# Optimization experiments

Hardware: AMD Instinct MI355X
Metric: run time of the kernel (lower is better)

Reference implementation:

```python
import jax, jax.numpy as jnp
import numpy as np
import math

B, L, D, H = 2, 2048, 1024, 16
DK = D // H


def setup_inputs() -> dict:
    key = jax.random.key(0)
    ks = jax.random.split(key, 11)
    s = 1.0 / math.sqrt(D)
    inp = {
        "query": jax.random.normal(ks[0], (B, L, D), jnp.float32),
        "key": jax.random.normal(ks[1], (B, L, D), jnp.float32),
        "value": jax.random.normal(ks[2], (B, L, D), jnp.float32),
        # mask == True (==1) means masked-out; causal mask over future positions
        "mask": jnp.triu(jnp.ones((L, L), dtype=bool), k=1),
        "Wq": jax.random.normal(ks[3], (D, D), jnp.float32) * s,
        "bq": jnp.zeros((D,), jnp.float32),
        "Wk": jax.random.normal(ks[4], (D, D), jnp.float32) * s,
        "bk": jnp.zeros((D,), jnp.float32),
        "Wv": jax.random.normal(ks[5], (D, D), jnp.float32) * s,
        "bv": jnp.zeros((D,), jnp.float32),
        "Wo": jax.random.normal(ks[6], (D, D), jnp.float32) * s,
        "bo": jnp.zeros((D,), jnp.float32),
    }
    return inp


def reference(query, key, value, mask, Wq, bq, Wk, bk, Wv, bv, Wo, bo):
    # Linear projections, then split heads: [B, L, D] -> [B, H, L, DK]
    def proj(x, W, b):
        return (x @ W.T + b).reshape(B, -1, H, DK).transpose(0, 2, 1, 3)

    Q = proj(query, Wq, bq)
    K = proj(key, Wk, bk)
    V = proj(value, Wv, bv)

    scale = 1.0 / math.sqrt(DK)
    scores = jnp.einsum("bhqd,bhkd->bhqk", Q, K) * scale  # [B,H,Lq,Lk]
    scores = jnp.where(mask, -jnp.inf, scores)
    attn = jax.nn.softmax(scores, axis=-1)  # dropout p=0 (eval mode)
    out = jnp.einsum("bhqk,bhkd->bhqd", attn, V)
    out = out.transpose(0, 2, 1, 3).reshape(B, -1, D)  # merge heads
    return out @ Wo.T + bo
```

## Files before the change

kernel.cpp:

```cpp
#include <hip/hip_runtime.h>
#include <hip/hip_bf16.h>
#include <math.h>

#define NL 2048
#define ND 1024

typedef __attribute__((ext_vector_type(8))) __bf16 bf16x8;
typedef __attribute__((ext_vector_type(4))) float f32x4;
typedef __attribute__((ext_vector_type(16))) float f32x16;
typedef __attribute__((ext_vector_type(4))) short short4v;
typedef __attribute__((ext_vector_type(2))) unsigned uint2v;
typedef __attribute__((ext_vector_type(4))) unsigned uint4v;

__device__ __forceinline__ short f2bf(float f) {
    union { float f; unsigned u; } v; v.f = f;
    unsigned u = v.u;
    u += 0x7FFF + ((u >> 16) & 1);
    return (short)(u >> 16);
}

__device__ __forceinline__ unsigned cvtpk2(float lo, float hi) {
    unsigned r;
    asm("v_cvt_pk_bf16_f32 %0, %1, %2" : "=v"(r) : "v"(lo), "v"(hi));
    return r;
}

__device__ __forceinline__ void gload16(const short* g, short* l) {
    __builtin_amdgcn_global_load_lds(
        (const __attribute__((address_space(1))) void*)g,
        (__attribute__((address_space(3))) void*)l, 16, 0, 0);
}

__global__ __launch_bounds__(256) void cvt_all(
    const float* __restrict__ q, const float* __restrict__ k, const float* __restrict__ v,
    const float* __restrict__ wq, const float* __restrict__ wk, const float* __restrict__ wv,
    short* __restrict__ xq, short* __restrict__ xk, short* __restrict__ xv,
    short* __restrict__ wbf) {
    const int bid = blockIdx.x;
    const float* src;
    short* dst;
    int blk;
    if (bid < 6144) {
        const int t = bid >> 11;
        src = t == 0 ? q : t == 1 ? k : v;
        dst = t == 0 ? xq : t == 1 ? xk : xv;
        blk = bid & 2047;
    } else {
        const int b2 = bid - 6144;
        const int t = b2 >> 9;
        src = t == 0 ? wq : t == 1 ? wk : wv;
        dst = wbf + (size_t)t * (1 << 20);
        blk = b2 & 511;
    }
    const int i = blk * 2048 + threadIdx.x * 8;
    f32x4 v0 = *(const f32x4*)&src[i];
    f32x4 v1 = *(const f32x4*)&src[i + 4];
    uint4v u = { cvtpk2(v0[0], v0[1]), cvtpk2(v0[2], v0[3]),
                 cvtpk2(v1[0], v1[1]), cvtpk2(v1[2], v1[3]) };
    *(uint4v*)&dst[i] = u;
}

__global__ __launch_bounds__(256) void cvt1(const float* __restrict__ src,
                                            short* __restrict__ dst) {
    const int i = blockIdx.x * 2048 + threadIdx.x * 8;
    f32x4 v0 = *(const f32x4*)&src[i];
    f32x4 v1 = *(const f32x4*)&src[i + 4];
    uint4v u = { cvtpk2(v0[0], v0[1]), cvtpk2(v0[2], v0[3]),
                 cvtpk2(v1[0], v1[1]), cvtpk2(v1[2], v1[3]) };
    *(uint4v*)&dst[i] = u;
}

__device__ __forceinline__ void gemm_core(const short* gA, const short* gB,
                                          short (*As)[4096], short (*Bs)[4096],
                                          int w, int wr, int wc, int lr, int lc,
                                          f32x4 acc[4][4]) {
    gload16(gA,         &As[0][w * 512]);
    gload16(gA + 65536, &As[0][w * 512 + 2048]);
    gload16(gB,         &Bs[0][w * 512]);
    gload16(gB + 65536, &Bs[0][w * 512 + 2048]);
    gload16(gA + 32,         &As[1][w * 512]);
    gload16(gA + 65536 + 32, &As[1][w * 512 + 2048]);
    gload16(gB + 32,         &Bs[1][w * 512]);
    gload16(gB + 65536 + 32, &Bs[1][w * 512 + 2048]);

    for (int t = 0; t < 30; ++t) {
        const int ws_ = (t + 2) & 3, rd = t & 3;
        const int k2 = (t + 2) * 32;
        gload16(gA + k2,         &As[ws_][w * 512]);
        gload16(gA + 65536 + k2, &As[ws_][w * 512 + 2048]);
        gload16(gB + k2,         &Bs[ws_][w * 512]);
        gload16(gB + 65536 + k2, &Bs[ws_][w * 512 + 2048]);
        asm volatile("s_waitcnt vmcnt(8)" ::: "memory");
        __builtin_amdgcn_s_barrier();
        asm volatile("" ::: "memory");

        bf16x8 a[4], b[4];
        #pragma unroll
        for (int mt = 0; mt < 4; ++mt)
            a[mt] = *(const bf16x8*)&As[rd][(wr * 64 + mt * 16 + lc) * 32 + lr * 8];
        #pragma unroll
        for (int nt = 0; nt < 4; ++nt)
            b[nt] = *(const bf16x8*)&Bs[rd][(wc * 64 + nt * 16 + lc) * 32 + lr * 8];
        __builtin_amdgcn_s_setprio(1);
        #pragma unroll
        for (int mt = 0; mt < 4; ++mt)
            #pragma unroll
            for (int nt = 0; nt < 4; ++nt)
                acc[mt][nt] = __builtin_amdgcn_mfma_f32_16x16x32_bf16(
                    a[mt], b[nt], acc[mt][nt], 0, 0, 0);
        __builtin_amdgcn_s_setprio(0);
    }
    #pragma unroll
    for (int pt = 0; pt < 2; ++pt) {
        if (pt == 0) asm volatile("s_waitcnt vmcnt(4)" ::: "memory");
        else         asm volatile("s_waitcnt vmcnt(0)" ::: "memory");
        __builtin_amdgcn_s_barrier();
        asm volatile("" ::: "memory");
        const int rd = 2 + pt;
        bf16x8 a[4], b[4];
        #pragma unroll
        for (int mt = 0; mt < 4; ++mt)
            a[mt] = *(const bf16x8*)&As[rd][(wr * 64 + mt * 16 + lc) * 32 + lr * 8];
        #pragma unroll
        for (int nt = 0; nt < 4; ++nt)
            b[nt] = *(const bf16x8*)&Bs[rd][(wc * 64 + nt * 16 + lc) * 32 + lr * 8];
        #pragma unroll
        for (int mt = 0; mt < 4; ++mt)
            #pragma unroll
            for (int nt = 0; nt < 4; ++nt)
                acc[mt][nt] = __builtin_amdgcn_mfma_f32_16x16x32_bf16(
                    a[mt], b[nt], acc[mt][nt], 0, 0, 0);
    }
}

__global__ __launch_bounds__(256) void gemm_qk(
    const short* __restrict__ Xqb, const short* __restrict__ Xkb,
    const short* __restrict__ Wqb, const short* __restrict__ Wkb,
    const float* __restrict__ bq, const float* __restrict__ bk,
    short* __restrict__ oq, short* __restrict__ ok) {
    __shared__ alignas(16) short As[4][4096];
    __shared__ alignas(16) short Bs[4][4096];

    const int bid  = blockIdx.x;
    const int xcd  = bid & 7, slot = bid >> 3;
    const int panel = xcd * 8 + (slot >> 3);
    const int zz   = panel >> 5;
    const int m0   = (panel & 31) * 128;
    const int n0   = (slot & 7) * 128;

    const short* Ab = zz ? Xkb : Xqb;
    const short* Wb = zz ? Wkb : Wqb;
    const float* bi = zz ? bk : bq;
    short* outp     = zz ? ok : oq;
    const float scl = zz ? 1.0f : 0.125f * 1.44269504088896f;

    const int tid = threadIdx.x, lane = tid & 63, w = tid >> 6;
    const int wr = w >> 1, wc = w & 1, lr = lane >> 4, lc = lane & 15;

    const short* gA = &Ab[(m0 + w * 16 + (lane >> 2)) * 1024 + (lane & 3) * 8];
    const short* gB = &Wb[(n0 + w * 16 + (lane >> 2)) * 1024 + (lane & 3) * 8];

    f32x4 acc[4][4] = {};
    gemm_core(gA, gB, As, Bs, w, wr, wc, lr, lc, acc);

    #pragma unroll
    for (int mt = 0; mt < 4; ++mt)
        #pragma unroll
        for (int nt = 0; nt < 4; ++nt)
            #pragma unroll
            for (int r = 0; r < 4; ++r) {
                int grow = m0 + wr * 64 + mt * 16 + lr * 4 + r;
                int gcol = n0 + wc * 64 + nt * 16 + lc;
                float val = (acc[mt][nt][r] + bi[gcol]) * scl;
                int bh = (grow >> 11) * 16 + (gcol >> 6);
                int q  = grow & 2047;
                int dk = gcol & 63;
                size_t addr = (size_t)bh * 131072 + (size_t)(q >> 5) * 2048 +
                              (dk >> 4) * 512 + ((dk >> 3) & 1) * 256 +
                              (q & 31) * 8 + (dk & 7);
                outp[addr] = f2bf(val);
            }
}

__global__ __launch_bounds__(256) void gemm_v(
    const short* __restrict__ Xvb, const short* __restrict__ Wvb,
    const float* __restrict__ bv, short* __restrict__ ov) {
    __shared__ alignas(16) short As[4][4096];
    __shared__ alignas(16) short Bs[4][4096];

    const int bid = blockIdx.x;
    const int xcd = bid & 7, slot = bid >> 3;
    const int m0  = (xcd * 4 + (slot >> 3)) * 128;
    const int n0  = (slot & 7) * 128;

    const int tid = threadIdx.x, lane = tid & 63, w = tid >> 6;
    const int wr = w >> 1, wc = w & 1, lr = lane >> 4, lc = lane & 15;

    const short* gA = &Xvb[(m0 + w * 16 + (lane >> 2)) * 1024 + (lane & 3) * 8];
    const short* gB = &Wvb[(n0 + w * 16 + (lane >> 2)) * 1024 + (lane & 3) * 8];

    f32x4 acc[4][4] = {};
    gemm_core(gA, gB, As, Bs, w, wr, wc, lr, lc, acc);

    #pragma unroll
    for (int mt = 0; mt < 4; ++mt)
        #pragma unroll
        for (int nt = 0; nt < 4; ++nt)
            #pragma unroll
            for (int r = 0; r < 4; ++r) {
                int grow = m0 + wr * 64 + mt * 16 + lr * 4 + r;
                int gcol = n0 + wc * 64 + nt * 16 + lc;
                float val = acc[mt][nt][r] + bv[gcol];
                int bh = (grow >> 11) * 16 + (gcol >> 6);
                int q  = grow & 2047;
                int dk = gcol & 63;
                size_t addr = (size_t)bh * 131072 + (size_t)(q >> 6) * 4096 +
                              ((q >> 4) & 3) * 1024 + (dk >> 5) * 512 +
                              ((q >> 3) & 1) * 256 + (dk & 31) * 8 + (q & 7);
                ov[addr] = f2bf(val);
            }
}

__global__ __launch_bounds__(256) void gemm_out(const short* __restrict__ Abf,
                                                const short* __restrict__ Wob,
                                                const float* __restrict__ bo,
                                                float* __restrict__ out) {
    __shared__ alignas(16) short As[4][4096];
    __shared__ alignas(16) short Bs[4][4096];

    const int bid = blockIdx.x;
    const int xcd = bid & 7, slot = bid >> 3;
    const int m0  = (xcd * 4 + (slot >> 3)) * 128;
    const int n0  = (slot & 7) * 128;

    const int tid = threadIdx.x, lane = tid & 63, w = tid >> 6;
    const int wr = w >> 1, wc = w & 1, lr = lane >> 4, lc = lane & 15;

    const short* gA = &Abf[(m0 + w * 16 + (lane >> 2)) * 1024 + (lane & 3) * 8];
    const short* gB = &Wob[(n0 + w * 16 + (lane >> 2)) * 1024 + (lane & 3) * 8];

    f32x4 acc[4][4] = {};
    gemm_core(gA, gB, As, Bs, w, wr, wc, lr, lc, acc);

    #pragma unroll
    for (int mt = 0; mt < 4; ++mt)
        #pragma unroll
        for (int nt = 0; nt < 4; ++nt)
            #pragma unroll
            for (int r = 0; r < 4; ++r) {
                int grow = m0 + wr * 64 + mt * 16 + lr * 4 + r;
                int gcol = n0 + wc * 64 + nt * 16 + lc;
                out[grow * 1024 + gcol] = acc[mt][nt][r] + bo[gcol];
            }
}

__global__ __launch_bounds__(256) void flash_attn(const short* __restrict__ Q,
                                                  const short* __restrict__ K,
                                                  const short* __restrict__ Vt,
                                                  short* __restrict__ AO) {
    __shared__ float mrg[2][64][49];

    const int tid  = threadIdx.x;
    const int lane = tid & 63;
    const int w    = tid >> 6;
    const int ql   = lane & 31;
    const int hi   = lane >> 5;

    const int bid  = blockIdx.x;
    const int xcd  = bid & 7;
    const int idx  = bid >> 3;
    const int bh   = xcd * 4 + (idx & 3);
    const int t    = 63 - (idx >> 2);
    const int q0   = t * 32;
    const int qa   = q0 + ql;
    const int nkb  = (t >> 1) + 1;
    const int kb_lo = (w * nkb) >> 2;
    const int kb_hi = ((w + 1) * nkb) >> 2;

    const short* Qp = Q  + (size_t)bh * 131072 + (size_t)t * 2048 + lane * 8;
    const short* Kp = K  + (size_t)bh * 131072 + lane * 8;
    const short* Vp = Vt + (size_t)bh * 131072 + lane * 8;

    bf16x8 qf[4];
    #pragma unroll
    for (int ks = 0; ks < 4; ++ks)
        qf[ks] = *(const bf16x8*)&Qp[ks * 512];

    f32x16 ot0 = {}, ot1 = {}, lacc = {};

    for (int kb = kb_lo; kb < kb_hi; ++kb) {
        bf16x8 kf[8];
        #pragma unroll
        for (int ks = 0; ks < 4; ++ks) {
            kf[2 * ks]     = *(const bf16x8*)&Kp[(size_t)(2 * kb) * 2048 + ks * 512];
            kf[2 * ks + 1] = *(const bf16x8*)&Kp[(size_t)(2 * kb + 1) * 2048 + ks * 512];
        }
        bf16x8 vf[8];
        #pragma unroll
        for (int ks = 0; ks < 4; ++ks) {
            vf[2 * ks]     = *(const bf16x8*)&Vp[(size_t)kb * 4096 + ks * 1024];
            vf[2 * ks + 1] = *(const bf16x8*)&Vp[(size_t)kb * 4096 + ks * 1024 + 512];
        }

        f32x16 st0 = {}, st1 = {};
        __builtin_amdgcn_s_setprio(1);
        #pragma unroll
        for (int ks = 0; ks < 4; ++ks) {
            st0 = __builtin_amdgcn_mfma_f32_32x32x16_bf16(kf[2 * ks],     qf[ks], st0, 0, 0, 0);
            st1 = __builtin_amdgcn_mfma_f32_32x32x16_bf16(kf[2 * ks + 1], qf[ks], st1, 0, 0, 0);
        }
        __builtin_amdgcn_s_setprio(0);

        if (kb == nkb - 1) {
            const int kv0 = kb * 64;
            #pragma unroll
            for (int r = 0; r < 16; ++r) {
                const int cr = (r & 3) + 8 * (r >> 2) + 4 * hi;
                if (kv0 + cr > qa)      st0[r] = -3.0e38f;
                if (kv0 + 32 + cr > qa) st1[r] = -3.0e38f;
            }
        }

        #pragma unroll
        for (int r = 0; r < 16; ++r) {
            st0[r] = exp2f(st0[r]);
            st1[r] = exp2f(st1[r]);
            lacc[r] += st0[r] + st1[r];
        }

        bf16x8 pf[4];
        #pragma unroll
        for (int blk = 0; blk < 2; ++blk) {
            const f32x16 s = blk ? st1 : st0;
            #pragma unroll
            for (int pks = 0; pks < 2; ++pks) {
                const int b = pks * 8;
                unsigned xa = cvtpk2(s[b + 0], s[b + 1]);
                unsigned xb = cvtpk2(s[b + 2], s[b + 3]);
                unsigned ya = cvtpk2(s[b + 4], s[b + 5]);
                unsigned yb = cvtpk2(s[b + 6], s[b + 7]);
                uint2v s0 = __builtin_amdgcn_permlane32_swap(xa, ya, false, false);
                uint2v s1 = __builtin_amdgcn_permlane32_swap(xb, yb, false, false);
                union { unsigned u[4]; bf16x8 v; } pu;
                pu.u[0] = s0[0]; pu.u[1] = s1[0]; pu.u[2] = s0[1]; pu.u[3] = s1[1];
                pf[blk * 2 + pks] = pu.v;
            }
        }

        __builtin_amdgcn_s_setprio(1);
        #pragma unroll
        for (int ks = 0; ks < 4; ++ks) {
            ot0 = __builtin_amdgcn_mfma_f32_32x32x16_bf16(vf[2 * ks],     pf[ks], ot0, 0, 0, 0);
            ot1 = __builtin_amdgcn_mfma_f32_32x32x16_bf16(vf[2 * ks + 1], pf[ks], ot1, 0, 0, 0);
        }
        __builtin_amdgcn_s_setprio(0);
    }

    if (w >= 2) {
        float* m = &mrg[w - 2][lane][0];
        #pragma unroll
        for (int r = 0; r < 16; ++r) {
            m[r] = ot0[r]; m[16 + r] = ot1[r]; m[32 + r] = lacc[r];
        }
    }
    __syncthreads();
    if (w < 2) {
        const float* m = &mrg[w][lane][0];
        #pragma unroll
        for (int r = 0; r < 16; ++r) {
            ot0[r] += m[r]; ot1[r] += m[16 + r]; lacc[r] += m[32 + r];
        }
    }
    if (w == 1) {
        float* m = &mrg[1][lane][0];
        #pragma unroll
        for (int r = 0; r < 16; ++r) {
            m[r] = ot0[r]; m[16 + r] = ot1[r]; m[32 + r] = lacc[r];
        }
    }
    __syncthreads();
    if (w == 0) {
        const float* m = &mrg[1][lane][0];
        #pragma unroll
        for (int r = 0; r < 16; ++r) {
            ot0[r] += m[r]; ot1[r] += m[16 + r]; lacc[r] += m[32 + r];
        }
        float sm[16];
        #pragma unroll
        for (int r = 0; r < 16; ++r) sm[r] = lacc[r];
        #pragma unroll
        for (int s = 8; s > 0; s >>= 1)
            #pragma unroll
            for (int i = 0; i < s; ++i) sm[i] += sm[i + s];
        const float l = sm[0] + __shfl_xor(sm[0], 32);
        const float inv = 1.f / l;

        const int b_ = bh >> 4, h_ = bh & 15;
        short* aoRow = AO + ((size_t)(b_ * NL + qa)) * ND + h_ * 64;
        #pragma unroll
        for (int db = 0; db < 2; ++db) {
            const f32x16 o = db ? ot1 : ot0;
            #pragma unroll
            for (int g = 0; g < 4; ++g) {
                short4v sv;
                #pragma unroll
                for (int i = 0; i < 4; ++i) sv[i] = f2bf(o[g * 4 + i] * inv);
                *(short4v*)&aoRow[db * 32 + g * 8 + 4 * hi] = sv;
            }
        }
    }
}

extern "C" void kernel_launch(void* const* d_in, const int* in_sizes, int n_in,
                              void* d_out, int out_size, void* d_ws, size_t ws_size,
                              hipStream_t stream) {
    const float* query = (const float*)d_in[0];
    const float* key   = (const float*)d_in[1];
    const float* value = (const float*)d_in[2];
    const float* Wq = (const float*)d_in[4];
    const float* bq = (const float*)d_in[5];
    const float* Wk = (const float*)d_in[6];
    const float* bk = (const float*)d_in[7];
    const float* Wv = (const float*)d_in[8];
    const float* bv = (const float*)d_in[9];
    const float* Wo = (const float*)d_in[10];
    const float* bo = (const float*)d_in[11];

    short* ws    = (short*)d_ws;
    short* dob   = (short*)d_out;
    short* q_ws  = ws;
    short* k_ws  = ws + (4 << 20);
    short* xq    = ws + (8 << 20);
    short* vt_ws = ws + (8 << 20);
    short* wbf   = ws + (12 << 20);
    short* ao_ws = ws + (12 << 20);
    short* wobf  = ws;
    short* xk    = dob;
    short* xv    = dob + (4 << 20);

    cvt_all<<<dim3(7680), 256, 0, stream>>>(query, key, value, Wq, Wk, Wv,
                                            xq, xk, xv, wbf);
    gemm_qk<<<dim3(512), 256, 0, stream>>>(xq, xk, wbf, wbf + (1 << 20),
                                           bq, bk, q_ws, k_ws);
    gemm_v<<<dim3(256), 256, 0, stream>>>(xv, wbf + (2 << 20), bv, vt_ws);
    flash_attn<<<dim3(2048), dim3(256), 0, stream>>>(q_ws, k_ws, vt_ws, ao_ws);
    cvt1<<<dim3(512), 256, 0, stream>>>(Wo, wobf);
    gemm_out<<<dim3(256), 256, 0, stream>>>(ao_ws, wobf, bo, (float*)d_out);
}
```

Baseline: 134.6 us.

## Split flash attention KV range over two waves with K double-buffering

```diff
diff --git a/kernel.cpp b/kernel.cpp
--- a/kernel.cpp
+++ b/kernel.cpp
@@ -254,11 +254,11 @@
             }
 }
 
-__global__ __launch_bounds__(256) void flash_attn(const short* __restrict__ Q,
-                                                  const short* __restrict__ K,
-                                                  const short* __restrict__ Vt,
-                                                  short* __restrict__ AO) {
-    __shared__ float mrg[2][64][49];
+__global__ __launch_bounds__(128, 3) void flash_attn(const short* __restrict__ Q,
+                                                     const short* __restrict__ K,
+                                                     const short* __restrict__ Vt,
+                                                     short* __restrict__ AO) {
+    __shared__ float mrg[64][49];
 
     const int tid  = threadIdx.x;
     const int lane = tid & 63;
@@ -274,8 +274,9 @@
     const int q0   = t * 32;
     const int qa   = q0 + ql;
     const int nkb  = (t >> 1) + 1;
-    const int kb_lo = (w * nkb) >> 2;
-    const int kb_hi = ((w + 1) * nkb) >> 2;
+    const int nkb2 = nkb >> 1;
+    const int kb_lo = w == 0 ? 0 : nkb2;
+    const int kb_hi = w == 0 ? nkb2 : nkb;
 
     const short* Qp = Q  + (size_t)bh * 131072 + (size_t)t * 2048 + lane * 8;
     const short* Kp = K  + (size_t)bh * 131072 + lane * 8;
@@ -288,102 +289,112 @@
 
     f32x16 ot0 = {}, ot1 = {}, lacc = {};
 
-    for (int kb = kb_lo; kb < kb_hi; ++kb) {
-        bf16x8 kf[8];
-        #pragma unroll
-        for (int ks = 0; ks < 4; ++ks) {
-            kf[2 * ks]     = *(const bf16x8*)&Kp[(size_t)(2 * kb) * 2048 + ks * 512];
-            kf[2 * ks + 1] = *(const bf16x8*)&Kp[(size_t)(2 * kb + 1) * 2048 + ks * 512];
-        }
-        bf16x8 vf[8];
-        #pragma unroll
-        for (int ks = 0; ks < 4; ++ks) {
-            vf[2 * ks]     = *(const bf16x8*)&Vp[(size_t)kb * 4096 + ks * 1024];
-            vf[2 * ks + 1] = *(const bf16x8*)&Vp[(size_t)kb * 4096 + ks * 1024 + 512];
-        }
-
-        f32x16 st0 = {}, st1 = {};
-        __builtin_amdgcn_s_setprio(1);
-        #pragma unroll
-        for (int ks = 0; ks < 4; ++ks) {
-            st0 = __builtin_amdgcn_mfma_f32_32x32x16_bf16(kf[2 * ks],     qf[ks], st0, 0, 0, 0);
-            st1 = __builtin_amdgcn_mfma_f32_32x32x16_bf16(kf[2 * ks + 1], qf[ks], st1, 0, 0, 0);
-        }
-        __builtin_amdgcn_s_setprio(0);
-
-        if (kb == nkb - 1) {
-            const int kv0 = kb * 64;
-            #pragma unroll
-            for (int r = 0; r < 16; ++r) {
-                const int cr = (r & 3) + 8 * (r >> 2) + 4 * hi;
-                if (kv0 + cr > qa)      st0[r] = -3.0e38f;
-                if (kv0 + 32 + cr > qa) st1[r] = -3.0e38f;
+#define LOADK(KF, KB)                                                          \
+    {                                                                          \
+        _Pragma("unroll")                                                      \
+        for (int ks = 0; ks < 4; ++ks) {                                       \
+            KF[2 * ks]     = *(const bf16x8*)&Kp[(size_t)(2 * (KB)) * 2048 + ks * 512];     \
+            KF[2 * ks + 1] = *(const bf16x8*)&Kp[(size_t)(2 * (KB) + 1) * 2048 + ks * 512]; \
+        }                                                                      \
+    }
+
+#define COMPUTE(KF, KB)                                                        \
+    {                                                                          \
+        f32x16 st0 = {}, st1 = {};                                             \
+        __builtin_amdgcn_s_setprio(1);                                         \
+        _Pragma("unroll")                                                      \
+        for (int ks = 0; ks < 4; ++ks) {                                       \
+            st0 = __builtin_amdgcn_mfma_f32_32x32x16_bf16(KF[2 * ks],     qf[ks], st0, 0, 0, 0); \
+            st1 = __builtin_amdgcn_mfma_f32_32x32x16_bf16(KF[2 * ks + 1], qf[ks], st1, 0, 0, 0); \
+        }                                                                      \
+        __builtin_amdgcn_s_setprio(0);                                         \
+        bf16x8 vf[8];                                                          \
+        _Pragma("unroll")                                                      \
+        for (int ks = 0; ks < 4; ++ks) {                                       \
+            vf[2 * ks]     = *(const bf16x8*)&Vp[(size_t)(KB) * 4096 + ks * 1024];       \
+            vf[2 * ks + 1] = *(const bf16x8*)&Vp[(size_t)(KB) * 4096 + ks * 1024 + 512]; \
+        }                                                                      \
+        if ((KB) == nkb - 1) {                                                 \
+            const int kv0 = (KB) * 64;                                         \
+            _Pragma("unroll")                                                  \
+            for (int r = 0; r < 16; ++r) {                                     \
+                const int cr = (r & 3) + 8 * (r >> 2) + 4 * hi;                \
+                if (kv0 + cr > qa)      st0[r] = -3.0e38f;                     \
+                if (kv0 + 32 + cr > qa) st1[r] = -3.0e38f;                     \
+            }                                                                  \
+        }                                                                      \
+        _Pragma("unroll")                                                      \
+        for (int r = 0; r < 16; ++r) {                                         \
+            st0[r] = exp2f(st0[r]);                                            \
+            st1[r] = exp2f(st1[r]);                                            \
+            lacc[r] += st0[r] + st1[r];                                        \
+        }                                                                      \
+        bf16x8 pf[4];                                                          \
+        _Pragma("unroll")                                                      \
+        for (int blk = 0; blk < 2; ++blk) {                                    \
+            const f32x16 s = blk ? st1 : st0;                                  \
+            _Pragma("unroll")                                                  \
+            for (int pks = 0; pks < 2; ++pks) {                                \
+                const int b = pks * 8;                                         \
+                unsigned xa = cvtpk2(s[b + 0], s[b + 1]);                      \
+                unsigned xb = cvtpk2(s[b + 2], s[b + 3]);                      \
+                unsigned ya = cvtpk2(s[b + 4], s[b + 5]);                      \
+                unsigned yb = cvtpk2(s[b + 6], s[b + 7]);                      \
+                uint2v s0 = __builtin_amdgcn_permlane32_swap(xa, ya, false, false); \
+                uint2v s1 = __builtin_amdgcn_permlane32_swap(xb, yb, false, false); \
+                union { unsigned u[4]; bf16x8 v; } pu;                         \
+                pu.u[0] = s0[0]; pu.u[1] = s1[0]; pu.u[2] = s0[1]; pu.u[3] = s1[1]; \
+                pf[blk * 2 + pks] = pu.v;                                      \
+            }                                                                  \
+        }                                                                      \
+        __builtin_amdgcn_s_setprio(1);                                         \
+        _Pragma("unroll")                                                      \
+        for (int ks = 0; ks < 4; ++ks) {                                       \
+            ot0 = __builtin_amdgcn_mfma_f32_32x32x16_bf16(vf[2 * ks],     pf[ks], ot0, 0, 0, 0); \
+            ot1 = __builtin_amdgcn_mfma_f32_32x32x16_bf16(vf[2 * ks + 1], pf[ks], ot1, 0, 0, 0); \
+        }                                                                      \
+        __builtin_amdgcn_s_setprio(0);                                         \
+    }
+
+    if (kb_lo < kb_hi) {
+        bf16x8 k0_[8], k1_[8];
+        int kb = kb_lo;
+        LOADK(k0_, kb);
+        while (kb + 1 < kb_hi) {
+            LOADK(k1_, kb + 1);
+            COMPUTE(k0_, kb);
+            ++kb;
+            if (kb + 1 < kb_hi) {
+                LOADK(k0_, kb + 1);
+                COMPUTE(k1_, kb);
+                ++kb;
+            } else {
+                COMPUTE(k1_, kb);
+                ++kb;
             }
         }
-
+        if (kb < kb_hi) {
+            COMPUTE(k0_, kb);
+        }
+    }
+#undef LOADK
+#undef COMPUTE
+
+    if (w == 0) {
         #pragma unroll
         for (int r = 0; r < 16; ++r) {
-            st0[r] = exp2f(st0[r]);
-            st1[r] = exp2f(st1[r]);
-            lacc[r] += st0[r] + st1[r];
+            mrg[lane][r]      = ot0[r];
+            mrg[lane][16 + r] = ot1[r];
+            mrg[lane][32 + r] = lacc[r];
         }
-
-        bf16x8 pf[4];
-        #pragma unroll
-        for (int blk = 0; blk < 2; ++blk) {
-            const f32x16 s = blk ? st1 : st0;
-            #pragma unroll
-            for (int pks = 0; pks < 2; ++pks) {
-                const int b = pks * 8;
-                unsigned xa = cvtpk2(s[b + 0], s[b + 1]);
-                unsigned xb = cvtpk2(s[b + 2], s[b + 3]);
-                unsigned ya = cvtpk2(s[b + 4], s[b + 5]);
-                unsigned yb = cvtpk2(s[b + 6], s[b + 7]);
-                uint2v s0 = __builtin_amdgcn_permlane32_swap(xa, ya, false, false);
-                uint2v s1 = __builtin_amdgcn_permlane32_swap(xb, yb, false, false);
-                union { unsigned u[4]; bf16x8 v; } pu;
-                pu.u[0] = s0[0]; pu.u[1] = s1[0]; pu.u[2] = s0[1]; pu.u[3] = s1[1];
-                pf[blk * 2 + pks] = pu.v;
-            }
-        }
-
-        __builtin_amdgcn_s_setprio(1);
-        #pragma unroll
-        for (int ks = 0; ks < 4; ++ks) {
-            ot0 = __builtin_amdgcn_mfma_f32_32x32x16_bf16(vf[2 * ks],     pf[ks], ot0, 0, 0, 0);
-            ot1 = __builtin_amdgcn_mfma_f32_32x32x16_bf16(vf[2 * ks + 1], pf[ks], ot1, 0, 0, 0);
-        }
-        __builtin_amdgcn_s_setprio(0);
-    }
-
-    if (w >= 2) {
-        float* m = &mrg[w - 2][lane][0];
+    }
+    __syncthreads();
+    if (w == 1) {
         #pragma unroll
         for (int r = 0; r < 16; ++r) {
-            m[r] = ot0[r]; m[16 + r] = ot1[r]; m[32 + r] = lacc[r];
-        }
-    }
-    __syncthreads();
-    if (w < 2) {
-        const float* m = &mrg[w][lane][0];
-        #pragma unroll
-        for (int r = 0; r < 16; ++r) {
-            ot0[r] += m[r]; ot1[r] += m[16 + r]; lacc[r] += m[32 + r];
-        }
-    }
-    if (w == 1) {
-        float* m = &mrg[1][lane][0];
-        #pragma unroll
-        for (int r = 0; r < 16; ++r) {
-            m[r] = ot0[r]; m[16 + r] = ot1[r]; m[32 + r] = lacc[r];
-        }
-    }
-    __syncthreads();
-    if (w == 0) {
-        const float* m = &mrg[1][lane][0];
-        #pragma unroll
-        for (int r = 0; r < 16; ++r) {
-            ot0[r] += m[r]; ot1[r] += m[16 + r]; lacc[r] += m[32 + r];
+            ot0[r]  += mrg[lane][r];
+            ot1[r]  += mrg[lane][16 + r];
+            lacc[r] += mrg[lane][32 + r];
         }
         float sm[16];
         #pragma unroll
@@ -443,7 +454,7 @@
     gemm_qk<<<dim3(512), 256, 0, stream>>>(xq, xk, wbf, wbf + (1 << 20),
                                            bq, bk, q_ws, k_ws);
     gemm_v<<<dim3(256), 256, 0, stream>>>(xv, wbf + (2 << 20), bv, vt_ws);
-    flash_attn<<<dim3(2048), dim3(256), 0, stream>>>(q_ws, k_ws, vt_ws, ao_ws);
+    flash_attn<<<dim3(2048), dim3(128), 0, stream>>>(q_ws, k_ws, vt_ws, ao_ws);
     cvt1<<<dim3(512), 256, 0, stream>>>(Wo, wobf);
     gemm_out<<<dim3(256), 256, 0, stream>>>(ao_ws, wobf, bo, (float*)d_out);
 }
```

New measurement: 202.1 us. 1.5x slower.
